# Optimization experiments

Measured on AMD Instinct MI355X. Metric: run time of the kernel, lower is better.

The kernel has to match this reference:

```python
import jax, jax.numpy as jnp
import numpy as np

V, H_BASE, D, L, K = 32000, 4096, 512, 2, 4
B = 64

def setup_inputs() -> dict:
    key = jax.random.key(0)
    ks = jax.random.split(key, 12)
    s = 0.02
    return {
        "hidden_state": jax.random.normal(ks[0], (B, H_BASE), jnp.float32),
        "in_proj_w": jax.random.normal(ks[1], (D, H_BASE), jnp.float32) * s,
        "in_proj_b": jnp.zeros((D,), jnp.float32),
        "w_ih0": jax.random.normal(ks[2], (3 * D, D), jnp.float32) * s,
        "w_hh0": jax.random.normal(ks[3], (3 * D, D), jnp.float32) * s,
        "b_ih0": jax.random.normal(ks[4], (3 * D,), jnp.float32) * s,
        "b_hh0": jax.random.normal(ks[5], (3 * D,), jnp.float32) * s,
        "w_ih1": jax.random.normal(ks[6], (3 * D, D), jnp.float32) * s,
        "w_hh1": jax.random.normal(ks[7], (3 * D, D), jnp.float32) * s,
        "b_ih1": jax.random.normal(ks[8], (3 * D,), jnp.float32) * s,
        "b_hh1": jax.random.normal(ks[9], (3 * D,), jnp.float32) * s,
        "embed": jax.random.normal(ks[10], (V, D), jnp.float32) * s,
        "out_w": jax.random.normal(ks[11], (V, D), jnp.float32) * s,
    }

def _gru_cell(x, h, w_ih, w_hh, b_ih, b_hh):
    # PyTorch GRU gate order: r, z, n
    gi = x @ w_ih.T + b_ih  # [B, 3D]
    gh = h @ w_hh.T + b_hh
    ir, iz, inn = jnp.split(gi, 3, axis=-1)
    hr, hz, hn = jnp.split(gh, 3, axis=-1)
    r = jax.nn.sigmoid(ir + hr)
    z = jax.nn.sigmoid(iz + hz)
    n = jnp.tanh(inn + r * hn)
    return (1.0 - z) * n + z * h

def reference(hidden_state, in_proj_w, in_proj_b, w_ih0, w_hh0, b_ih0, b_hh0,
              w_ih1, w_hh1, b_ih1, b_hh1, embed, out_w):
    b = hidden_state.shape[0]
    h0 = hidden_state @ in_proj_w.T + in_proj_b  # [B, D]
    h_l0 = h0
    h_l1 = h0
    x = jnp.zeros((b, in_proj_w.shape[0]), hidden_state.dtype)
    all_logits = []
    for _ in range(K):
        h_l0 = _gru_cell(x, h_l0, w_ih0, w_hh0, b_ih0, b_hh0)
        h_l1 = _gru_cell(h_l0, h_l1, w_ih1, w_hh1, b_ih1, b_hh1)
        logits = h_l1 @ out_w.T  # [B, V]
        all_logits.append(logits)
        x = embed[jnp.argmax(logits, axis=-1)]  # greedy next-token embed
    return jnp.stack(all_logits, axis=1)  # [B, K, V]
```

## Files before the change

kernel.cpp:

```cpp
#include <hip/hip_runtime.h>
#include <math.h>


typedef __attribute__((ext_vector_type(8))) short short8;
typedef __attribute__((ext_vector_type(4))) float f32x4;

__device__ __forceinline__ unsigned short f2bf_rne(float x) {
    unsigned u = __float_as_uint(x);
    unsigned r = (u + 0x7fffu + ((u >> 16) & 1u)) >> 16;
    return (unsigned short)r;
}
__device__ __forceinline__ void split2(float x, unsigned short& hi, unsigned short& lo) {
    unsigned u = __float_as_uint(x);
    hi = (unsigned short)(u >> 16);
    float r = x - __uint_as_float(u & 0xffff0000u);
    lo = f2bf_rne(r);
}

__device__ __forceinline__ void store_plane(unsigned short* hiP, unsigned short* loP,
                                            int m, int d, float v) {
    int s = d >> 6, cl = (d >> 3) & 7, e = d & 7;
    int off = m * 512 + s * 64 + ((cl ^ (m & 7)) * 8) + e;
    unsigned short hi, lo; split2(v, hi, lo);
    hiP[off] = hi; loP[off] = lo;
}

__device__ __forceinline__ void gload16(const void* g, void* lds) {
    __builtin_amdgcn_global_load_lds(
        (const __attribute__((address_space(1))) unsigned int*)g,
        (__attribute__((address_space(3))) unsigned int*)lds, 16, 0, 0);
}

__device__ __forceinline__ void split_w_body(
    const float* __restrict__ W, unsigned short* __restrict__ H,
    unsigned short* __restrict__ L, size_t g, int kclog)
{
    int n  = (int)(g >> kclog);
    int c8 = (int)g & ((1 << kclog) - 1);
    const float* src = W + g * 8;
    float4 v0 = *(const float4*)src;
    float4 v1 = *(const float4*)(src + 4);
    unsigned short h[8], l[8];
    split2(v0.x,h[0],l[0]); split2(v0.y,h[1],l[1]); split2(v0.z,h[2],l[2]); split2(v0.w,h[3],l[3]);
    split2(v1.x,h[4],l[4]); split2(v1.y,h[5],l[5]); split2(v1.z,h[6],l[6]); split2(v1.w,h[7],l[7]);
    uint4 ph = make_uint4((unsigned)h[0]|((unsigned)h[1]<<16), (unsigned)h[2]|((unsigned)h[3]<<16),
                          (unsigned)h[4]|((unsigned)h[5]<<16), (unsigned)h[6]|((unsigned)h[7]<<16));
    uint4 pl = make_uint4((unsigned)l[0]|((unsigned)l[1]<<16), (unsigned)l[2]|((unsigned)l[3]<<16),
                          (unsigned)l[4]|((unsigned)l[5]<<16), (unsigned)l[6]|((unsigned)l[7]<<16));
    int nt = n >> 7, row = n & 127;
    int ksi = c8 >> 3;
    int slot = (c8 & 7) ^ (row & 7);
    int tpr = 1 << (kclog - 3);
    size_t off = ((size_t)(nt * tpr + ksi) * 128 + row) * 64 + slot * 8;
    *(uint4*)(H + off) = ph;
    *(uint4*)(L + off) = pl;
}

__device__ __forceinline__ void split_a_body(
    const float* __restrict__ hidden, char* __restrict__ hidH,
    char* __restrict__ hidL, int g)
{
    int m = g >> 9;
    int cc = g & 511;
    int s = cc >> 3, cl = cc & 7;
    const float* src = hidden + m * 4096 + cc * 8;
    float4 v0 = *(const float4*)src;
    float4 v1 = *(const float4*)(src + 4);
    unsigned short h[8], l[8];
    split2(v0.x,h[0],l[0]); split2(v0.y,h[1],l[1]); split2(v0.z,h[2],l[2]); split2(v0.w,h[3],l[3]);
    split2(v1.x,h[4],l[4]); split2(v1.y,h[5],l[5]); split2(v1.z,h[6],l[6]); split2(v1.w,h[7],l[7]);
    uint4 ph = make_uint4((unsigned)h[0]|((unsigned)h[1]<<16), (unsigned)h[2]|((unsigned)h[3]<<16),
                          (unsigned)h[4]|((unsigned)h[5]<<16), (unsigned)h[6]|((unsigned)h[7]<<16));
    uint4 pl = make_uint4((unsigned)l[0]|((unsigned)l[1]<<16), (unsigned)l[2]|((unsigned)l[3]<<16),
                          (unsigned)l[4]|((unsigned)l[5]<<16), (unsigned)l[6]|((unsigned)l[7]<<16));
    int off = m * 8192 + s * 128 + ((cl ^ (m & 7)) * 16);
    *(uint4*)(hidH + off) = ph;
    *(uint4*)(hidL + off) = pl;
}

__device__ __forceinline__ void mfma_core(
    const unsigned short* __restrict__ AsH0, const unsigned short* __restrict__ AsL0,
    const unsigned short* __restrict__ BsH0, const unsigned short* __restrict__ BsL0,
    int wv, int lr, int lh, f32x4* acc)
{
#pragma unroll
    for (int kk2 = 0; kk2 < 2; ++kk2) {
        int aoff = lr * 64 + (((kk2 * 4 + lh) ^ (lr & 7)) * 8);
        short8 ah[4], al[4];
#pragma unroll
        for (int mt = 0; mt < 4; ++mt) {
            ah[mt] = *(const short8*)(AsH0 + mt * 1024 + aoff);
            al[mt] = *(const short8*)(AsL0 + mt * 1024 + aoff);
        }
        int brow = wv * 16 + lr;
        int boff = brow * 64 + (((kk2 * 4 + lh) ^ (brow & 7)) * 8);
        short8 bh = *(const short8*)(BsH0 + boff);
        short8 bl = *(const short8*)(BsL0 + boff);
#pragma unroll
        for (int mt = 0; mt < 4; ++mt) {
            acc[mt] = __builtin_amdgcn_mfma_f32_16x16x32_bf16(ah[mt], bh, acc[mt], 0, 0, 0);
            acc[mt] = __builtin_amdgcn_mfma_f32_16x16x32_bf16(ah[mt], bl, acc[mt], 0, 0, 0);
            acc[mt] = __builtin_amdgcn_mfma_f32_16x16x32_bf16(al[mt], bh, acc[mt], 0, 0, 0);
        }
    }
}

__device__ __forceinline__ void epilogue_write(
    float* __restrict__ C, int ldc, int n0, int wv, int lr, int lh, const f32x4* acc)
{
#pragma unroll
    for (int mt = 0; mt < 4; ++mt)
#pragma unroll
        for (int i = 0; i < 4; ++i) {
            int mm = mt * 16 + lh * 4 + i;
            C[mm * ldc + n0 + wv * 16 + lr] = acc[mt][i];
        }
}

__device__ __forceinline__ unsigned orderable(float v) {
    unsigned u = __float_as_uint(v);
    return (u & 0x80000000u) ? ~u : (u | 0x80000000u);
}

template<bool ARGMAX>
__device__ __forceinline__ void mfma_gemm(
    const char* __restrict__ AH, const char* __restrict__ AL, int AstrideB, int akk0,
    const unsigned short* __restrict__ BH, const unsigned short* __restrict__ BL,
    size_t btileU, int nk,
    float* __restrict__ C, int ldc, int n0,
    unsigned short (*AsH)[4096], unsigned short (*AsL)[4096],
    unsigned short (*BsH)[8192], unsigned short (*BsL)[8192],
    unsigned long long* __restrict__ packed)
{
    const int tid  = threadIdx.x;
    const int wv   = tid >> 6;
    const int lane = tid & 63;
    const int lr   = lane & 15;
    const int lh   = lane >> 4;
    const int m    = tid >> 3;
    const int cp   = tid & 7;

    f32x4 acc[4];
#pragma unroll
    for (int i = 0; i < 4; ++i) acc[i] = (f32x4){0.f, 0.f, 0.f, 0.f};

    auto stage = [&](int t, int p) {
        const int ka = (akk0 + t * 64) * 2;
        gload16(AH + m * AstrideB + ka + cp * 16, (char*)AsH[p] + wv * 1024);
        gload16(AL + m * AstrideB + ka + cp * 16, (char*)AsL[p] + wv * 1024);
        const char* bH = (const char*)BH + (btileU + (size_t)t * 8192) * 2;
        const char* bL = (const char*)BL + (btileU + (size_t)t * 8192) * 2;
        gload16(bH + wv * 2048 +        lane * 16, (char*)BsH[p] + wv * 2048);
        gload16(bH + wv * 2048 + 1024 + lane * 16, (char*)BsH[p] + wv * 2048 + 1024);
        gload16(bL + wv * 2048 +        lane * 16, (char*)BsL[p] + wv * 2048);
        gload16(bL + wv * 2048 + 1024 + lane * 16, (char*)BsL[p] + wv * 2048 + 1024);
    };

    stage(0, 0);
    __syncthreads();

    for (int t = 0; t < nk; ++t) {
        const int p = t & 1;
        if (t + 1 < nk) stage(t + 1, p ^ 1);
        mfma_core(AsH[p], AsL[p], BsH[p], BsL[p], wv, lr, lh, acc);
        __syncthreads();
    }

    epilogue_write(C, ldc, n0, wv, lr, lh, acc);

    if (ARGMAX) {
        float* sv = (float*)&AsH[0][0];
        int*   sc = (int*)&AsL[0][0];
#pragma unroll
        for (int mt = 0; mt < 4; ++mt)
#pragma unroll
            for (int i = 0; i < 4; ++i) {
                float v = acc[mt][i];
                int   c = n0 + wv * 16 + lr;
#pragma unroll
                for (int msk = 1; msk < 16; msk <<= 1) {
                    float ov = __shfl_xor(v, msk, 64);
                    int   oc = __shfl_xor(c, msk, 64);
                    if (ov > v || (ov == v && oc < c)) { v = ov; c = oc; }
                }
                if (lr == 0) {
                    int row = mt * 16 + lh * 4 + i;
                    sv[wv * 64 + row] = v;
                    sc[wv * 64 + row] = c;
                }
            }
        __syncthreads();
        if (tid < 64) {
            float v = sv[tid]; int c = sc[tid];
#pragma unroll
            for (int w = 1; w < 8; ++w) {
                float ov = sv[w * 64 + tid]; int oc = sc[w * 64 + tid];
                if (ov > v || (ov == v && oc < c)) { v = ov; c = oc; }
            }
            unsigned long long pk =
                ((unsigned long long)orderable(v) << 32) | (unsigned)(~(unsigned)c);
            atomicMax(packed + tid, pk);
        }
    }
}

#define DECLARE_LDS() \
    __shared__ alignas(16) unsigned short AsH[2][4096]; \
    __shared__ alignas(16) unsigned short AsL[2][4096]; \
    __shared__ alignas(16) unsigned short BsH[2][8192]; \
    __shared__ alignas(16) unsigned short BsL[2][8192];

__global__ __launch_bounds__(256) void k_split_all(
    const float* __restrict__ out_w, const float* __restrict__ w_ih0,
    const float* __restrict__ w_hh0, const float* __restrict__ w_ih1,
    const float* __restrict__ w_hh1, const float* __restrict__ in_w,
    const float* __restrict__ hidden,
    unsigned short* __restrict__ owH, unsigned short* __restrict__ owL,
    unsigned short* __restrict__ gwH, unsigned short* __restrict__ gwL,
    unsigned short* __restrict__ inH, unsigned short* __restrict__ inL,
    char* __restrict__ hidH, char* __restrict__ hidL)
{
    size_t gt = (size_t)blockIdx.x * 256 + threadIdx.x;
    for (size_t u = gt; u < 2736128; u += 524288) {
        if (u < 2048000) {
            split_w_body(out_w, owH, owL, u, 6);
        } else if (u < 2441216) {
            size_t g = u - 2048000;
            int mat = (int)(g / 98304);
            const float* W = mat == 0 ? w_ih0 : mat == 1 ? w_hh0
                           : mat == 2 ? w_ih1 : w_hh1;
            split_w_body(W, gwH + (size_t)mat * 786432, gwL + (size_t)mat * 786432,
                         g % 98304, 6);
        } else if (u < 2703360) {
            split_w_body(in_w, inH, inL, u - 2441216, 9);
        } else {
            split_a_body(hidden, hidH, hidL, (int)(u - 2703360));
        }
    }
}

__global__ __launch_bounds__(512) void k_inproj(
    const char* __restrict__ hidH, const char* __restrict__ hidL,
    const unsigned short* __restrict__ inH, const unsigned short* __restrict__ inL,
    float* __restrict__ ipart)
{
    DECLARE_LDS();
    int nt = blockIdx.x & 3;
    int ks = blockIdx.x >> 2;
    mfma_gemm<false>(hidH, hidL, 8192, ks * 64,
                     inH, inL, (size_t)(nt * 64 + ks) * 8192, 1,
                     ipart + ks * 32768, 512, nt * 128,
                     AsH, AsL, BsH, BsL, nullptr);
}

__global__ __launch_bounds__(512) void k_reduce_inproj(
    const float* __restrict__ ipart, const float* __restrict__ bias,
    float* __restrict__ hA0, float* __restrict__ hB,
    unsigned short* hAH, unsigned short* hAL,
    unsigned short* hBH, unsigned short* hBL)
{
    int i = blockIdx.x * 512 + threadIdx.x;
    int b = i >> 9;
    int d = i & 511;
    float s = bias[d];
#pragma unroll 8
    for (int ks = 0; ks < 64; ++ks) s += ipart[ks * 32768 + i];
    hA0[i] = s;
    hB[i] = s;
    store_plane(hAH, hAL, b, d, s);
    store_plane(hBH, hBL, b, d, s);
}

__global__ __launch_bounds__(512) void k_gh_init(
    const char* __restrict__ hAH, const char* __restrict__ hAL,
    const char* __restrict__ hBH, const char* __restrict__ hBL,
    const unsigned short* __restrict__ gwH, const unsigned short* __restrict__ gwL,
    float* __restrict__ gh0_b0, float* __restrict__ gh1)
{
    DECLARE_LDS();
    int bx = blockIdx.x;
    if (bx < 96) {
        int nt = bx % 12, ks = bx / 12;
        size_t btile = ((size_t)96 + nt * 8 + ks) * 8192;
        mfma_gemm<false>(hAH, hAL, 1024, ks * 64, gwH, gwL, btile, 1,
                         gh0_b0 + ks * 98304, 1536, nt * 128,
                         AsH, AsL, BsH, BsL, nullptr);
    } else {
        int idx = bx - 96;
        int nt = idx % 12, ks2 = idx / 12;
        size_t btile = ((size_t)288 + nt * 8 + ks2 * 2) * 8192;
        mfma_gemm<false>(hBH, hBL, 1024, ks2 * 128, gwH, gwL, btile, 2,
                         gh1 + ks2 * 98304, 1536, nt * 128,
                         AsH, AsL, BsH, BsL, nullptr);
    }
}

__global__ __launch_bounds__(512) void k_gi0(
    const unsigned long long* __restrict__ packed,
    const float* __restrict__ embed,
    const unsigned short* __restrict__ gwH, const unsigned short* __restrict__ gwL,
    float* __restrict__ gi0)
{
    DECLARE_LDS();
    const int tid = threadIdx.x;
    const int wv = tid >> 6, lane = tid & 63, lr = lane & 15, lh = lane >> 4;
    int nt = blockIdx.x % 12, ks = blockIdx.x / 12;

    size_t btileU = ((size_t)nt * 8 + ks) * 8192;
    const char* bH = (const char*)gwH + btileU * 2;
    const char* bL = (const char*)gwL + btileU * 2;
    gload16(bH + wv * 2048 +        lane * 16, (char*)BsH[0] + wv * 2048);
    gload16(bH + wv * 2048 + 1024 + lane * 16, (char*)BsH[0] + wv * 2048 + 1024);
    gload16(bL + wv * 2048 +        lane * 16, (char*)BsL[0] + wv * 2048);
    gload16(bL + wv * 2048 + 1024 + lane * 16, (char*)BsL[0] + wv * 2048 + 1024);

    {
        int mm = tid >> 3, cp = tid & 7;
        unsigned long long pk = packed[mm];
        int tok = (int)(~(unsigned)(pk & 0xffffffffu));
        const float* src = embed + (size_t)tok * 512 + ks * 64 + cp * 8;
        float4 v0 = *(const float4*)src;
        float4 v1 = *(const float4*)(src + 4);
        unsigned short h[8], l[8];
        split2(v0.x,h[0],l[0]); split2(v0.y,h[1],l[1]); split2(v0.z,h[2],l[2]); split2(v0.w,h[3],l[3]);
        split2(v1.x,h[4],l[4]); split2(v1.y,h[5],l[5]); split2(v1.z,h[6],l[6]); split2(v1.w,h[7],l[7]);
        uint4 ph = make_uint4((unsigned)h[0]|((unsigned)h[1]<<16), (unsigned)h[2]|((unsigned)h[3]<<16),
                              (unsigned)h[4]|((unsigned)h[5]<<16), (unsigned)h[6]|((unsigned)h[7]<<16));
        uint4 pl = make_uint4((unsigned)l[0]|((unsigned)l[1]<<16), (unsigned)l[2]|((unsigned)l[3]<<16),
                              (unsigned)l[4]|((unsigned)l[5]<<16), (unsigned)l[6]|((unsigned)l[7]<<16));
        int off = mm * 64 + ((cp ^ (mm & 7)) * 8);
        *(uint4*)(AsH[0] + off) = ph;
        *(uint4*)(AsL[0] + off) = pl;
    }
    __syncthreads();

    f32x4 acc[4];
#pragma unroll
    for (int i = 0; i < 4; ++i) acc[i] = (f32x4){0.f, 0.f, 0.f, 0.f};
    mfma_core(AsH[0], AsL[0], BsH[0], BsL[0], wv, lr, lh, acc);
    epilogue_write(gi0 + ks * 98304, 1536, nt * 128, wv, lr, lh, acc);
}

__global__ __launch_bounds__(512) void k_fused_l1(
    int step,
    const float* __restrict__ hA_cur, float* __restrict__ hA_nxt,
    const float* __restrict__ gi0,
    const float* __restrict__ gh0_cur, float* __restrict__ gh0_nxt,
    float* __restrict__ gi1,
    const unsigned short* __restrict__ gwH, const unsigned short* __restrict__ gwL,
    const float* __restrict__ b_ih0, const float* __restrict__ b_hh0)
{
    DECLARE_LDS();
    const int bx = blockIdx.x, tid = threadIdx.x;
    const int nt = bx % 12, ks = (bx / 12) & 7, mat = bx / 96;
    if (mat == 1 && step == 3) return;
    const int wv = tid >> 6, lane = tid & 63, lr = lane & 15, lh = lane >> 4;

    size_t btileU = ((size_t)(mat ? 96 : 192) + nt * 8 + ks) * 8192;
    const char* bH = (const char*)gwH + btileU * 2;
    const char* bL = (const char*)gwL + btileU * 2;
    gload16(bH + wv * 2048 +        lane * 16, (char*)BsH[0] + wv * 2048);
    gload16(bH + wv * 2048 + 1024 + lane * 16, (char*)BsH[0] + wv * 2048 + 1024);
    gload16(bL + wv * 2048 +        lane * 16, (char*)BsL[0] + wv * 2048);
    gload16(bL + wv * 2048 + 1024 + lane * 16, (char*)BsL[0] + wv * 2048 + 1024);

    {
        const int b = tid >> 3, cl = tid & 7;
        const int d0 = ks * 64 + cl * 8;
        float ir[8], iz[8], in_[8], hr[8], hz[8], hn[8];
        {
            float4 u0, u1;
            u0 = *(const float4*)(b_ih0 + d0);        u1 = *(const float4*)(b_ih0 + d0 + 4);
            ir[0]=u0.x; ir[1]=u0.y; ir[2]=u0.z; ir[3]=u0.w; ir[4]=u1.x; ir[5]=u1.y; ir[6]=u1.z; ir[7]=u1.w;
            u0 = *(const float4*)(b_ih0 + 512 + d0);  u1 = *(const float4*)(b_ih0 + 512 + d0 + 4);
            iz[0]=u0.x; iz[1]=u0.y; iz[2]=u0.z; iz[3]=u0.w; iz[4]=u1.x; iz[5]=u1.y; iz[6]=u1.z; iz[7]=u1.w;
            u0 = *(const float4*)(b_ih0 + 1024 + d0); u1 = *(const float4*)(b_ih0 + 1024 + d0 + 4);
            in_[0]=u0.x; in_[1]=u0.y; in_[2]=u0.z; in_[3]=u0.w; in_[4]=u1.x; in_[5]=u1.y; in_[6]=u1.z; in_[7]=u1.w;
            u0 = *(const float4*)(b_hh0 + d0);        u1 = *(const float4*)(b_hh0 + d0 + 4);
            hr[0]=u0.x; hr[1]=u0.y; hr[2]=u0.z; hr[3]=u0.w; hr[4]=u1.x; hr[5]=u1.y; hr[6]=u1.z; hr[7]=u1.w;
            u0 = *(const float4*)(b_hh0 + 512 + d0);  u1 = *(const float4*)(b_hh0 + 512 + d0 + 4);
            hz[0]=u0.x; hz[1]=u0.y; hz[2]=u0.z; hz[3]=u0.w; hz[4]=u1.x; hz[5]=u1.y; hz[6]=u1.z; hz[7]=u1.w;
            u0 = *(const float4*)(b_hh0 + 1024 + d0); u1 = *(const float4*)(b_hh0 + 1024 + d0 + 4);
            hn[0]=u0.x; hn[1]=u0.y; hn[2]=u0.z; hn[3]=u0.w; hn[4]=u1.x; hn[5]=u1.y; hn[6]=u1.z; hn[7]=u1.w;
        }
        if (step > 0) {
#pragma unroll
            for (int p = 0; p < 8; ++p) {
                const float* g = gi0 + p * 98304 + b * 1536 + d0;
                float4 a0, a1;
                a0 = *(const float4*)(g);        a1 = *(const float4*)(g + 4);
                ir[0]+=a0.x; ir[1]+=a0.y; ir[2]+=a0.z; ir[3]+=a0.w; ir[4]+=a1.x; ir[5]+=a1.y; ir[6]+=a1.z; ir[7]+=a1.w;
                a0 = *(const float4*)(g + 512);  a1 = *(const float4*)(g + 516);
                iz[0]+=a0.x; iz[1]+=a0.y; iz[2]+=a0.z; iz[3]+=a0.w; iz[4]+=a1.x; iz[5]+=a1.y; iz[6]+=a1.z; iz[7]+=a1.w;
                a0 = *(const float4*)(g + 1024); a1 = *(const float4*)(g + 1028);
                in_[0]+=a0.x; in_[1]+=a0.y; in_[2]+=a0.z; in_[3]+=a0.w; in_[4]+=a1.x; in_[5]+=a1.y; in_[6]+=a1.z; in_[7]+=a1.w;
            }
        }
#pragma unroll
        for (int p = 0; p < 8; ++p) {
            const float* g = gh0_cur + p * 98304 + b * 1536 + d0;
            float4 a0, a1;
            a0 = *(const float4*)(g);        a1 = *(const float4*)(g + 4);
            hr[0]+=a0.x; hr[1]+=a0.y; hr[2]+=a0.z; hr[3]+=a0.w; hr[4]+=a1.x; hr[5]+=a1.y; hr[6]+=a1.z; hr[7]+=a1.w;
            a0 = *(const float4*)(g + 512);  a1 = *(const float4*)(g + 516);
            hz[0]+=a0.x; hz[1]+=a0.y; hz[2]+=a0.z; hz[3]+=a0.w; hz[4]+=a1.x; hz[5]+=a1.y; hz[6]+=a1.z; hz[7]+=a1.w;
            a0 = *(const float4*)(g + 1024); a1 = *(const float4*)(g + 1028);
            hn[0]+=a0.x; hn[1]+=a0.y; hn[2]+=a0.z; hn[3]+=a0.w; hn[4]+=a1.x; hn[5]+=a1.y; hn[6]+=a1.z; hn[7]+=a1.w;
        }
        float hold[8];
        {
            float4 u0 = *(const float4*)(hA_cur + b * 512 + d0);
            float4 u1 = *(const float4*)(hA_cur + b * 512 + d0 + 4);
            hold[0]=u0.x; hold[1]=u0.y; hold[2]=u0.z; hold[3]=u0.w;
            hold[4]=u1.x; hold[5]=u1.y; hold[6]=u1.z; hold[7]=u1.w;
        }
        float hv[8];
        unsigned short hh[8], ll[8];
#pragma unroll
        for (int e = 0; e < 8; ++e) {
            float r = 1.f / (1.f + expf(-(ir[e] + hr[e])));
            float z = 1.f / (1.f + expf(-(iz[e] + hz[e])));
            float n = tanhf(in_[e] + r * hn[e]);
            hv[e] = (1.f - z) * n + z * hold[e];
            split2(hv[e], hh[e], ll[e]);
        }
        uint4 ph = make_uint4((unsigned)hh[0]|((unsigned)hh[1]<<16), (unsigned)hh[2]|((unsigned)hh[3]<<16),
                              (unsigned)hh[4]|((unsigned)hh[5]<<16), (unsigned)hh[6]|((unsigned)hh[7]<<16));
        uint4 pl = make_uint4((unsigned)ll[0]|((unsigned)ll[1]<<16), (unsigned)ll[2]|((unsigned)ll[3]<<16),
                              (unsigned)ll[4]|((unsigned)ll[5]<<16), (unsigned)ll[6]|((unsigned)ll[7]<<16));
        int off = b * 64 + ((cl ^ (b & 7)) * 8);
        *(uint4*)(AsH[0] + off) = ph;
        *(uint4*)(AsL[0] + off) = pl;
        if (mat == 0 && nt == 0) {
            *(float4*)(hA_nxt + b * 512 + d0)     = make_float4(hv[0], hv[1], hv[2], hv[3]);
            *(float4*)(hA_nxt + b * 512 + d0 + 4) = make_float4(hv[4], hv[5], hv[6], hv[7]);
        }
    }
    __syncthreads();

    f32x4 acc[4];
#pragma unroll
    for (int i = 0; i < 4; ++i) acc[i] = (f32x4){0.f, 0.f, 0.f, 0.f};
    mfma_core(AsH[0], AsL[0], BsH[0], BsL[0], wv, lr, lh, acc);
    epilogue_write((mat ? gh0_nxt : gi1) + ks * 98304, 1536, nt * 128, wv, lr, lh, acc);
}

__global__ __launch_bounds__(512) void k_combine1(
    const float* __restrict__ gi1, const float* __restrict__ gh1,
    const float* __restrict__ b_ih, const float* __restrict__ b_hh,
    float* __restrict__ hB, unsigned short* hBH, unsigned short* hBL,
    unsigned long long* __restrict__ packed)
{
    int i = blockIdx.x * 512 + threadIdx.x;
    int b = i >> 9;
    int d = i & 511;
    int base = b * 1536 + d;
    float ir = b_ih[d], iz = b_ih[d + 512], inn = b_ih[d + 1024];
    float hr = b_hh[d], hz = b_hh[d + 512], hn = b_hh[d + 1024];
#pragma unroll
    for (int ks = 0; ks < 8; ++ks) {
        const float* g = gi1 + ks * 98304 + base;
        ir += g[0]; iz += g[512]; inn += g[1024];
    }
#pragma unroll
    for (int ks = 0; ks < 4; ++ks) {
        const float* g = gh1 + ks * 98304 + base;
        hr += g[0]; hz += g[512]; hn += g[1024];
    }
    float r = 1.f / (1.f + expf(-(ir + hr)));
    float z = 1.f / (1.f + expf(-(iz + hz)));
    float n = tanhf(inn + r * hn);
    float hv = (1.f - z) * n + z * hB[i];
    hB[i] = hv;
    store_plane(hBH, hBL, b, d, hv);
    if (blockIdx.x == 0 && threadIdx.x < 64) packed[threadIdx.x] = 0ull;
}

__global__ __launch_bounds__(512) void k_logits_gh1(
    const char* __restrict__ hBH, const char* __restrict__ hBL,
    const unsigned short* __restrict__ owH, const unsigned short* __restrict__ owL,
    const unsigned short* __restrict__ gwH, const unsigned short* __restrict__ gwL,
    float* __restrict__ out, int step,
    unsigned long long* __restrict__ packed, float* __restrict__ gh1)
{
    DECLARE_LDS();
    int bx = blockIdx.x;
    if (bx < 48) {
        if (step == 3) return;
        int nt = bx % 12, ks2 = bx / 12;
        size_t btile = ((size_t)288 + nt * 8 + ks2 * 2) * 8192;
        mfma_gemm<false>(hBH, hBL, 1024, ks2 * 128, gwH, gwL, btile, 2,
                         gh1 + ks2 * 98304, 1536, nt * 128,
                         AsH, AsL, BsH, BsL, nullptr);
    } else {
        int lx = bx - 48;
        mfma_gemm<true>(hBH, hBL, 1024, 0, owH, owL, (size_t)lx * 8 * 8192, 8,
                        out + step * 32000, 128000, lx * 128,
                        AsH, AsL, BsH, BsL, packed);
    }
}

extern "C" void kernel_launch(void* const* d_in, const int* in_sizes, int n_in,
                              void* d_out, int out_size, void* d_ws, size_t ws_size,
                              hipStream_t stream)
{
    const float* hidden = (const float*)d_in[0];
    const float* in_w   = (const float*)d_in[1];
    const float* in_b   = (const float*)d_in[2];
    const float* w_ih0  = (const float*)d_in[3];
    const float* w_hh0  = (const float*)d_in[4];
    const float* b_ih0  = (const float*)d_in[5];
    const float* b_hh0  = (const float*)d_in[6];
    const float* w_ih1  = (const float*)d_in[7];
    const float* w_hh1  = (const float*)d_in[8];
    const float* b_ih1  = (const float*)d_in[9];
    const float* b_hh1  = (const float*)d_in[10];
    const float* embed  = (const float*)d_in[11];
    const float* out_w  = (const float*)d_in[12];
    float* out = (float*)d_out;
    char*  ws  = (char*)d_ws;

    float* hA0 = (float*)(ws + 0);
    float* hA1 = (float*)(ws + 131072);
    float* hB  = (float*)(ws + 262144);
    unsigned short* hAH = (unsigned short*)(ws + 393216);
    unsigned short* hAL = (unsigned short*)(ws + 458752);
    unsigned short* hBH = (unsigned short*)(ws + 524288);
    unsigned short* hBL = (unsigned short*)(ws + 589824);
    char* hidH = ws + 655360;
    char* hidL = ws + 1179648;
    float* gi0    = (float*)(ws + 1703936);
    float* gh0b0  = (float*)(ws + 4849664);
    float* gh0b1  = (float*)(ws + 7995392);
    float* gi1    = (float*)(ws + 11141120);
    float* gh1    = (float*)(ws + 14286848);
    unsigned long long* packed = (unsigned long long*)(ws + 15859712);
    float* ipart  = (float*)(ws + 15863808);
    unsigned short* owH = (unsigned short*)(ws + 24252416);
    unsigned short* owL = (unsigned short*)(ws + 57020416);
    unsigned short* gwH = (unsigned short*)(ws + 89788416);
    unsigned short* gwL = (unsigned short*)(ws + 96079872);
    unsigned short* inH = (unsigned short*)(ws + 102371328);
    unsigned short* inL = (unsigned short*)(ws + 106565632);

    k_split_all<<<2048, 256, 0, stream>>>(out_w, w_ih0, w_hh0, w_ih1, w_hh1,
                                          in_w, hidden,
                                          owH, owL, gwH, gwL, inH, inL, hidH, hidL);
    k_inproj<<<256, 512, 0, stream>>>(hidH, hidL, inH, inL, ipart);
    k_reduce_inproj<<<64, 512, 0, stream>>>(ipart, in_b, hA0, hB,
                                            hAH, hAL, hBH, hBL);
    k_gh_init<<<144, 512, 0, stream>>>((char*)hAH, (char*)hAL,
                                       (char*)hBH, (char*)hBL,
                                       gwH, gwL, gh0b0, gh1);

    float* hA_bufs[2] = { hA0, hA1 };
    float* gh0_bufs[2] = { gh0b0, gh0b1 };
    for (int step = 0; step < 4; ++step) {
        if (step > 0)
            k_gi0<<<96, 512, 0, stream>>>(packed, embed, gwH, gwL, gi0);
        k_fused_l1<<<192, 512, 0, stream>>>(step,
                                            hA_bufs[step & 1], hA_bufs[(step + 1) & 1],
                                            gi0,
                                            gh0_bufs[step & 1], gh0_bufs[(step + 1) & 1],
                                            gi1, gwH, gwL, b_ih0, b_hh0);
        k_combine1<<<64, 512, 0, stream>>>(gi1, gh1, b_ih1, b_hh1,
                                           hB, hBH, hBL, packed);
        k_logits_gh1<<<298, 512, 0, stream>>>((char*)hBH, (char*)hBL,
                                              owH, owL, gwH, gwL,
                                              out, step, packed, gh1);
    }
}
```

Measured before the change: 399.3 us.

## Split out_w into bf16 hi/lo planes on the fly inside the logits kernel

The separate pre-pass that converted the whole 32000x512 output projection into bf16 hi/lo planes in workspace is removed. The logits kernel now loads fp32 out_w rows directly, splits them in registers and writes swizzled planes into LDS, overlapping the next tile's load with the current MFMA work. The aim is to avoid the extra full-size read/write of the converted planes. The logits/gh1 kernel is also retiled to 64-column tiles with 256 threads and twice the blocks. The trade-off is that the split ALU work is repeated in each of the four steps, and the per-block argmax reduction now spans four waves instead of eight.

```diff
diff --git a/kernel.cpp b/kernel.cpp
--- a/kernel.cpp
+++ b/kernel.cpp
@@ -122,15 +122,13 @@
     return (u & 0x80000000u) ? ~u : (u | 0x80000000u);
 }
 
-template<bool ARGMAX>
-__device__ __forceinline__ void mfma_gemm(
+__device__ __forceinline__ void mfma_gemm8(
     const char* __restrict__ AH, const char* __restrict__ AL, int AstrideB, int akk0,
     const unsigned short* __restrict__ BH, const unsigned short* __restrict__ BL,
     size_t btileU, int nk,
     float* __restrict__ C, int ldc, int n0,
     unsigned short (*AsH)[4096], unsigned short (*AsL)[4096],
-    unsigned short (*BsH)[8192], unsigned short (*BsL)[8192],
-    unsigned long long* __restrict__ packed)
+    unsigned short (*BsH)[8192], unsigned short (*BsL)[8192])
 {
     const int tid  = threadIdx.x;
     const int wv   = tid >> 6;
@@ -167,41 +165,6 @@
     }
 
     epilogue_write(C, ldc, n0, wv, lr, lh, acc);
-
-    if (ARGMAX) {
-        float* sv = (float*)&AsH[0][0];
-        int*   sc = (int*)&AsL[0][0];
-#pragma unroll
-        for (int mt = 0; mt < 4; ++mt)
-#pragma unroll
-            for (int i = 0; i < 4; ++i) {
-                float v = acc[mt][i];
-                int   c = n0 + wv * 16 + lr;
-#pragma unroll
-                for (int msk = 1; msk < 16; msk <<= 1) {
-                    float ov = __shfl_xor(v, msk, 64);
-                    int   oc = __shfl_xor(c, msk, 64);
-                    if (ov > v || (ov == v && oc < c)) { v = ov; c = oc; }
-                }
-                if (lr == 0) {
-                    int row = mt * 16 + lh * 4 + i;
-                    sv[wv * 64 + row] = v;
-                    sc[wv * 64 + row] = c;
-                }
-            }
-        __syncthreads();
-        if (tid < 64) {
-            float v = sv[tid]; int c = sc[tid];
-#pragma unroll
-            for (int w = 1; w < 8; ++w) {
-                float ov = sv[w * 64 + tid]; int oc = sc[w * 64 + tid];
-                if (ov > v || (ov == v && oc < c)) { v = ov; c = oc; }
-            }
-            unsigned long long pk =
-                ((unsigned long long)orderable(v) << 32) | (unsigned)(~(unsigned)c);
-            atomicMax(packed + tid, pk);
-        }
-    }
 }
 
 #define DECLARE_LDS() \
@@ -211,31 +174,24 @@
     __shared__ alignas(16) unsigned short BsL[2][8192];
 
 __global__ __launch_bounds__(256) void k_split_all(
-    const float* __restrict__ out_w, const float* __restrict__ w_ih0,
-    const float* __restrict__ w_hh0, const float* __restrict__ w_ih1,
-    const float* __restrict__ w_hh1, const float* __restrict__ in_w,
-    const float* __restrict__ hidden,
-    unsigned short* __restrict__ owH, unsigned short* __restrict__ owL,
+    const float* __restrict__ w_ih0, const float* __restrict__ w_hh0,
+    const float* __restrict__ w_ih1, const float* __restrict__ w_hh1,
+    const float* __restrict__ in_w, const float* __restrict__ hidden,
     unsigned short* __restrict__ gwH, unsigned short* __restrict__ gwL,
     unsigned short* __restrict__ inH, unsigned short* __restrict__ inL,
     char* __restrict__ hidH, char* __restrict__ hidL)
 {
-    size_t gt = (size_t)blockIdx.x * 256 + threadIdx.x;
-    for (size_t u = gt; u < 2736128; u += 524288) {
-        if (u < 2048000) {
-            split_w_body(out_w, owH, owL, u, 6);
-        } else if (u < 2441216) {
-            size_t g = u - 2048000;
-            int mat = (int)(g / 98304);
-            const float* W = mat == 0 ? w_ih0 : mat == 1 ? w_hh0
-                           : mat == 2 ? w_ih1 : w_hh1;
-            split_w_body(W, gwH + (size_t)mat * 786432, gwL + (size_t)mat * 786432,
-                         g % 98304, 6);
-        } else if (u < 2703360) {
-            split_w_body(in_w, inH, inL, u - 2441216, 9);
-        } else {
-            split_a_body(hidden, hidH, hidL, (int)(u - 2703360));
-        }
+    size_t u = (size_t)blockIdx.x * 256 + threadIdx.x;
+    if (u < 393216) {
+        int mat = (int)(u / 98304);
+        const float* W = mat == 0 ? w_ih0 : mat == 1 ? w_hh0
+                       : mat == 2 ? w_ih1 : w_hh1;
+        split_w_body(W, gwH + (size_t)mat * 786432, gwL + (size_t)mat * 786432,
+                     u % 98304, 6);
+    } else if (u < 655360) {
+        split_w_body(in_w, inH, inL, u - 393216, 9);
+    } else {
+        split_a_body(hidden, hidH, hidL, (int)(u - 655360));
     }
 }
 
@@ -247,10 +203,10 @@
     DECLARE_LDS();
     int nt = blockIdx.x & 3;
     int ks = blockIdx.x >> 2;
-    mfma_gemm<false>(hidH, hidL, 8192, ks * 64,
-                     inH, inL, (size_t)(nt * 64 + ks) * 8192, 1,
-                     ipart + ks * 32768, 512, nt * 128,
-                     AsH, AsL, BsH, BsL, nullptr);
+    mfma_gemm8(hidH, hidL, 8192, ks * 64,
+               inH, inL, (size_t)(nt * 64 + ks) * 8192, 1,
+               ipart + ks * 32768, 512, nt * 128,
+               AsH, AsL, BsH, BsL);
 }
 
 __global__ __launch_bounds__(512) void k_reduce_inproj(
@@ -282,16 +238,16 @@
     if (bx < 96) {
         int nt = bx % 12, ks = bx / 12;
         size_t btile = ((size_t)96 + nt * 8 + ks) * 8192;
-        mfma_gemm<false>(hAH, hAL, 1024, ks * 64, gwH, gwL, btile, 1,
-                         gh0_b0 + ks * 98304, 1536, nt * 128,
-                         AsH, AsL, BsH, BsL, nullptr);
+        mfma_gemm8(hAH, hAL, 1024, ks * 64, gwH, gwL, btile, 1,
+                   gh0_b0 + ks * 98304, 1536, nt * 128,
+                   AsH, AsL, BsH, BsL);
     } else {
         int idx = bx - 96;
         int nt = idx % 12, ks2 = idx / 12;
         size_t btile = ((size_t)288 + nt * 8 + ks2 * 2) * 8192;
-        mfma_gemm<false>(hBH, hBL, 1024, ks2 * 128, gwH, gwL, btile, 2,
-                         gh1 + ks2 * 98304, 1536, nt * 128,
-                         AsH, AsL, BsH, BsL, nullptr);
+        mfma_gemm8(hBH, hBL, 1024, ks2 * 128, gwH, gwL, btile, 2,
+                   gh1 + ks2 * 98304, 1536, nt * 128,
+                   AsH, AsL, BsH, BsL);
     }
 }
 
@@ -476,27 +432,140 @@
     if (blockIdx.x == 0 && threadIdx.x < 64) packed[threadIdx.x] = 0ull;
 }
 
-__global__ __launch_bounds__(512) void k_logits_gh1(
+__global__ __launch_bounds__(256) void k_logits_gh1(
     const char* __restrict__ hBH, const char* __restrict__ hBL,
-    const unsigned short* __restrict__ owH, const unsigned short* __restrict__ owL,
+    const float* __restrict__ out_w,
     const unsigned short* __restrict__ gwH, const unsigned short* __restrict__ gwL,
     float* __restrict__ out, int step,
     unsigned long long* __restrict__ packed, float* __restrict__ gh1)
 {
-    DECLARE_LDS();
-    int bx = blockIdx.x;
-    if (bx < 48) {
+    __shared__ alignas(16) unsigned short AsH[2][4096];
+    __shared__ alignas(16) unsigned short AsL[2][4096];
+    __shared__ alignas(16) unsigned short BsH[2][4096];
+    __shared__ alignas(16) unsigned short BsL[2][4096];
+
+    const int tid  = threadIdx.x;
+    const int wv   = tid >> 6;
+    const int lane = tid & 63;
+    const int lr   = lane & 15;
+    const int lh   = lane >> 4;
+    const int bx   = blockIdx.x;
+
+    const int ar1 = wv * 16 + (lane >> 3);
+    const int acp = lane & 7;
+    auto stageA = [&](int kaB, int p) {
+        gload16(hBH + ar1 * 1024 + kaB + acp * 16,       (char*)AsH[p] + wv * 2048);
+        gload16(hBH + (ar1 + 8) * 1024 + kaB + acp * 16, (char*)AsH[p] + wv * 2048 + 1024);
+        gload16(hBL + ar1 * 1024 + kaB + acp * 16,       (char*)AsL[p] + wv * 2048);
+        gload16(hBL + (ar1 + 8) * 1024 + kaB + acp * 16, (char*)AsL[p] + wv * 2048 + 1024);
+    };
+
+    f32x4 acc[4];
+#pragma unroll
+    for (int i = 0; i < 4; ++i) acc[i] = (f32x4){0.f, 0.f, 0.f, 0.f};
+
+    if (bx < 96) {
         if (step == 3) return;
-        int nt = bx % 12, ks2 = bx / 12;
-        size_t btile = ((size_t)288 + nt * 8 + ks2 * 2) * 8192;
-        mfma_gemm<false>(hBH, hBL, 1024, ks2 * 128, gwH, gwL, btile, 2,
-                         gh1 + ks2 * 98304, 1536, nt * 128,
-                         AsH, AsL, BsH, BsL, nullptr);
-    } else {
-        int lx = bx - 48;
-        mfma_gemm<true>(hBH, hBL, 1024, 0, owH, owL, (size_t)lx * 8 * 8192, 8,
-                        out + step * 32000, 128000, lx * 128,
-                        AsH, AsL, BsH, BsL, packed);
+        const int nt2 = bx % 24, ks2 = bx / 24;
+        auto stageB = [&](int t, int p) {
+            size_t bu = ((size_t)288 + (nt2 >> 1) * 8 + ks2 * 2 + t) * 8192
+                      + (size_t)(nt2 & 1) * 4096;
+            const char* bH = (const char*)(gwH + bu);
+            const char* bL = (const char*)(gwL + bu);
+            gload16(bH + wv * 2048 +        lane * 16, (char*)BsH[p] + wv * 2048);
+            gload16(bH + wv * 2048 + 1024 + lane * 16, (char*)BsH[p] + wv * 2048 + 1024);
+            gload16(bL + wv * 2048 +        lane * 16, (char*)BsL[p] + wv * 2048);
+            gload16(bL + wv * 2048 + 1024 + lane * 16, (char*)BsL[p] + wv * 2048 + 1024);
+        };
+        stageA((ks2 * 128) * 2, 0);  stageB(0, 0);
+        __syncthreads();
+        stageA((ks2 * 128 + 64) * 2, 1);  stageB(1, 1);
+        mfma_core(AsH[0], AsL[0], BsH[0], BsL[0], wv, lr, lh, acc);
+        __syncthreads();
+        mfma_core(AsH[1], AsL[1], BsH[1], BsL[1], wv, lr, lh, acc);
+        epilogue_write(gh1 + ks2 * 98304, 1536, nt2 * 64, wv, lr, lh, acc);
+        return;
+    }
+
+    const int lx = bx - 96;
+    const int n0 = lx * 64;
+    const int bn = tid >> 2, bq = tid & 3;
+    const float* Wb = out_w + (size_t)(n0 + bn) * 512 + bq * 16;
+    const int wo0 = bn * 64 + (((2 * bq)     ^ (bn & 7)) * 8);
+    const int wo1 = bn * 64 + (((2 * bq + 1) ^ (bn & 7)) * 8);
+
+    float4 r0, r1, r2, r3;
+    auto loadB = [&](int t) {
+        const float* s = Wb + t * 64;
+        r0 = *(const float4*)s;       r1 = *(const float4*)(s + 4);
+        r2 = *(const float4*)(s + 8); r3 = *(const float4*)(s + 12);
+    };
+    auto writeB = [&](int p) {
+        unsigned short h[16], l[16];
+        split2(r0.x,h[0],l[0]);   split2(r0.y,h[1],l[1]);   split2(r0.z,h[2],l[2]);   split2(r0.w,h[3],l[3]);
+        split2(r1.x,h[4],l[4]);   split2(r1.y,h[5],l[5]);   split2(r1.z,h[6],l[6]);   split2(r1.w,h[7],l[7]);
+        split2(r2.x,h[8],l[8]);   split2(r2.y,h[9],l[9]);   split2(r2.z,h[10],l[10]); split2(r2.w,h[11],l[11]);
+        split2(r3.x,h[12],l[12]); split2(r3.y,h[13],l[13]); split2(r3.z,h[14],l[14]); split2(r3.w,h[15],l[15]);
+        *(uint4*)(BsH[p] + wo0) = make_uint4(
+            (unsigned)h[0]|((unsigned)h[1]<<16),  (unsigned)h[2]|((unsigned)h[3]<<16),
+            (unsigned)h[4]|((unsigned)h[5]<<16),  (unsigned)h[6]|((unsigned)h[7]<<16));
+        *(uint4*)(BsH[p] + wo1) = make_uint4(
+            (unsigned)h[8]|((unsigned)h[9]<<16),  (unsigned)h[10]|((unsigned)h[11]<<16),
+            (unsigned)h[12]|((unsigned)h[13]<<16),(unsigned)h[14]|((unsigned)h[15]<<16));
+        *(uint4*)(BsL[p] + wo0) = make_uint4(
+            (unsigned)l[0]|((unsigned)l[1]<<16),  (unsigned)l[2]|((unsigned)l[3]<<16),
+            (unsigned)l[4]|((unsigned)l[5]<<16),  (unsigned)l[6]|((unsigned)l[7]<<16));
+        *(uint4*)(BsL[p] + wo1) = make_uint4(
+            (unsigned)l[8]|((unsigned)l[9]<<16),  (unsigned)l[10]|((unsigned)l[11]<<16),
+            (unsigned)l[12]|((unsigned)l[13]<<16),(unsigned)l[14]|((unsigned)l[15]<<16));
+    };
+
+    loadB(0);
+    stageA(0, 0);
+    writeB(0);
+    __syncthreads();
+#pragma unroll
+    for (int t = 0; t < 8; ++t) {
+        const int p = t & 1;
+        if (t < 7) { loadB(t + 1); stageA((t + 1) * 128, p ^ 1); }
+        mfma_core(AsH[p], AsL[p], BsH[p], BsL[p], wv, lr, lh, acc);
+        if (t < 7) writeB(p ^ 1);
+        __syncthreads();
+    }
+
+    epilogue_write(out + step * 32000, 128000, n0, wv, lr, lh, acc);
+
+    float* sv = (float*)&AsH[0][0];
+    int*   sc = (int*)&AsL[0][0];
+#pragma unroll
+    for (int mt = 0; mt < 4; ++mt)
+#pragma unroll
+        for (int i = 0; i < 4; ++i) {
+            float v = acc[mt][i];
+            int   c = n0 + wv * 16 + lr;
+#pragma unroll
+            for (int msk = 1; msk < 16; msk <<= 1) {
+                float ov = __shfl_xor(v, msk, 64);
+                int   oc = __shfl_xor(c, msk, 64);
+                if (ov > v || (ov == v && oc < c)) { v = ov; c = oc; }
+            }
+            if (lr == 0) {
+                int row = mt * 16 + lh * 4 + i;
+                sv[wv * 64 + row] = v;
+                sc[wv * 64 + row] = c;
+            }
+        }
+    __syncthreads();
+    if (tid < 64) {
+        float v = sv[tid]; int c = sc[tid];
+#pragma unroll
+        for (int w = 1; w < 4; ++w) {
+            float ov = sv[w * 64 + tid]; int oc = sc[w * 64 + tid];
+            if (ov > v || (ov == v && oc < c)) { v = ov; c = oc; }
+        }
+        unsigned long long pk =
+            ((unsigned long long)orderable(v) << 32) | (unsigned)(~(unsigned)c);
+        atomicMax(packed + tid, pk);
     }
 }
 
@@ -536,16 +605,14 @@
     float* gh1    = (float*)(ws + 14286848);
     unsigned long long* packed = (unsigned long long*)(ws + 15859712);
     float* ipart  = (float*)(ws + 15863808);
-    unsigned short* owH = (unsigned short*)(ws + 24252416);
-    unsigned short* owL = (unsigned short*)(ws + 57020416);
-    unsigned short* gwH = (unsigned short*)(ws + 89788416);
-    unsigned short* gwL = (unsigned short*)(ws + 96079872);
-    unsigned short* inH = (unsigned short*)(ws + 102371328);
-    unsigned short* inL = (unsigned short*)(ws + 106565632);
-
-    k_split_all<<<2048, 256, 0, stream>>>(out_w, w_ih0, w_hh0, w_ih1, w_hh1,
+    unsigned short* gwH = (unsigned short*)(ws + 24252416);
+    unsigned short* gwL = (unsigned short*)(ws + 30543872);
+    unsigned short* inH = (unsigned short*)(ws + 36835328);
+    unsigned short* inL = (unsigned short*)(ws + 41029632);
+
+    k_split_all<<<2688, 256, 0, stream>>>(w_ih0, w_hh0, w_ih1, w_hh1,
                                           in_w, hidden,
-                                          owH, owL, gwH, gwL, inH, inL, hidH, hidL);
+                                          gwH, gwL, inH, inL, hidH, hidL);
     k_inproj<<<256, 512, 0, stream>>>(hidH, hidL, inH, inL, ipart);
     k_reduce_inproj<<<64, 512, 0, stream>>>(ipart, in_b, hA0, hB,
                                             hAH, hAL, hBH, hBL);
@@ -565,8 +632,8 @@
                                             gi1, gwH, gwL, b_ih0, b_hh0);
         k_combine1<<<64, 512, 0, stream>>>(gi1, gh1, b_ih1, b_hh1,
                                            hB, hBH, hBL, packed);
-        k_logits_gh1<<<298, 512, 0, stream>>>((char*)hBH, (char*)hBL,
-                                              owH, owL, gwH, gwL,
+        k_logits_gh1<<<596, 256, 0, stream>>>((char*)hBH, (char*)hBL,
+                                              out_w, gwH, gwL,
                                               out, step, packed, gh1);
     }
 }
```

Measured after the change: 406.2 us. About the same (+1.7%).
